# Performance work log

Measured on AMD Instinct MI355X. Metric: run time of the kernel, lower is better.

The kernel has to match this reference:

```python
import jax, jax.numpy as jnp
import numpy as np

B, S, K = 64, 80, 32          # patients, max visits, codes per visit
V, E, H, L = 10000, 256, 512, 128  # vocab, embed, hidden, latent


def setup_inputs() -> dict:
    key = jax.random.key(0)
    ks = jax.random.split(key, 9)
    input_sequence = jax.random.randint(ks[0], (B, S, K), 0, V)
    length = jax.random.randint(ks[1], (B,), 1, S + 1)  # valid lengths >= 1
    sc = 0.05
    embedding_weight = jax.random.normal(ks[2], (V, E), jnp.float32) * sc
    Wi = jax.random.normal(ks[3], (3 * H, E), jnp.float32) * sc   # W_ih (r,z,n)
    Wh = jax.random.normal(ks[4], (3 * H, H), jnp.float32) * sc   # W_hh (r,z,n)
    bi = jax.random.normal(ks[5], (3 * H,), jnp.float32) * sc
    bh = jax.random.normal(ks[6], (3 * H,), jnp.float32) * sc
    W_lat = jax.random.normal(ks[7], (L, H), jnp.float32) * sc
    b_lat = jax.random.normal(ks[8], (L,), jnp.float32) * sc
    return dict(input_sequence=input_sequence, length=length,
                embedding_weight=embedding_weight, Wi=Wi, Wh=Wh, bi=bi, bh=bh,
                W_lat=W_lat, b_lat=b_lat)


def _encode(input_sequence, length, embedding_weight, Wi, Wh, bi, bh, W_lat, b_lat):
    b, s, k = input_sequence.shape
    v, e = embedding_weight.shape
    h = Wh.shape[1]
    # torch.sort(length, descending=True) -> batch reorder (output stays sorted!)
    sorted_idx = jnp.argsort(-length)
    sorted_len = length[sorted_idx]
    seq = input_sequence[sorted_idx]
    # multi-hot scatter: duplicates collapse to 1, matching torch scatter_(dim=2, val=1)
    onehot = jnp.zeros((b, s, v), jnp.float32)
    onehot = onehot.at[jnp.arange(b)[:, None, None],
                       jnp.arange(s)[None, :, None], seq].set(1.0)
    onehot = onehot.at[:, :, 0].set(0.0)  # code 0 is padding
    emb = jnp.tanh(jnp.einsum('bsv,ve->bse', onehot, embedding_weight))  # [B,S,E]
    # packed GRU == masked scan: hidden frozen once t >= length
    mask = jnp.arange(s)[None, :] < sorted_len[:, None]  # [B,S]
    xs = jnp.swapaxes(emb, 0, 1)   # [S,B,E]
    ms = jnp.swapaxes(mask, 0, 1)  # [S,B]

    def step(hprev, xm):
        x, m = xm
        gi = x @ Wi.T + bi        # [B,3H]
        gh = hprev @ Wh.T + bh    # [B,3H]
        i_r, i_z, i_n = jnp.split(gi, 3, axis=-1)
        h_r, h_z, h_n = jnp.split(gh, 3, axis=-1)
        r = jax.nn.sigmoid(i_r + h_r)
        z = jax.nn.sigmoid(i_z + h_z)
        n = jnp.tanh(i_n + r * h_n)
        hnew = (1.0 - z) * n + z * hprev
        return jnp.where(m[:, None], hnew, hprev), None

    h0 = jnp.zeros((b, h), jnp.float32)
    hT, _ = jax.lax.scan(step, h0, (xs, ms))  # last valid hidden per sequence
    return jnp.tanh(hT @ W_lat.T + b_lat)     # [B,L], in sorted order


def reference(input_sequence, length, embedding_weight, Wi, Wh, bi, bh, W_lat, b_lat):
    return _encode(input_sequence, length, embedding_weight, Wi, Wh, bi, bh, W_lat, b_lat)
```

## Files before the change

kernel.cpp:

```cpp
#include <hip/hip_runtime.h>
#include <cmath>

typedef _Float16 f16;
typedef _Float16 f16x8 __attribute__((ext_vector_type(8)));
typedef float f32x4 __attribute__((ext_vector_type(4)));
typedef unsigned int u32x4 __attribute__((ext_vector_type(4)));

#define B 64
#define S 80
#define KC 32
#define EDIM 256
#define HDIM 512
#define G3 1536
#define LDIM 128

#define NG 8
#define PG 8
#define NJ 16
#define CPB 32

#define OFF_PCNT  (NG * NJ * 64)
#define OFF_XCD   (OFF_PCNT + NG * 64)
#define OFF_TEST  (OFF_XCD + NG * NJ)
#define OFF_FAIL  (OFF_TEST + NG * NJ * 64)
#define SYNC_TOTAL (OFF_FAIL + NG)

__device__ __forceinline__ unsigned int ld_u32c(const unsigned int* p, bool l2) {
    unsigned int v;
    if (l2) {
        asm volatile("global_load_dword %0, %1, off sc0\n\ts_waitcnt vmcnt(0)"
                     : "=v"(v) : "v"(p) : "memory");
    } else {
        v = __hip_atomic_load(p, __ATOMIC_RELAXED, __HIP_MEMORY_SCOPE_AGENT);
    }
    return v;
}
__device__ __forceinline__ void st_u32c(unsigned int* p, unsigned int v, bool l2) {
    if (l2) {
        asm volatile("global_store_dword %0, %1, off sc0" :: "v"(p), "v"(v) : "memory");
    } else {
        __hip_atomic_store(p, v, __ATOMIC_RELAXED, __HIP_MEMORY_SCOPE_AGENT);
    }
}

__global__ __launch_bounds__(256) void emb_kernel(const int* __restrict__ seq,
                                                  const float* __restrict__ Ew,
                                                  unsigned short* __restrict__ emb16) {
    int bs = blockIdx.x;
    __shared__ int codes[KC];
    __shared__ int valid[KC];
    int tid = threadIdx.x;
    if (tid < KC) codes[tid] = seq[bs * KC + tid];
    __syncthreads();
    if (tid < KC) {
        int c = codes[tid];
        int v = (c != 0);
        for (int i = 0; i < tid; ++i)
            if (codes[i] == c) v = 0;
        valid[tid] = v;
    }
    __syncthreads();
    float acc = 0.f;
    for (int j = 0; j < KC; ++j) {
        if (valid[j]) acc += Ew[codes[j] * EDIM + tid];
    }
    emb16[bs * EDIM + tid] = __builtin_bit_cast(unsigned short, (f16)tanhf(acc));
}

__global__ __launch_bounds__(256) void gi_gemm16(
        const unsigned short* __restrict__ wi16,
        const unsigned short* __restrict__ emb16,
        const float* __restrict__ bi,
        unsigned short* __restrict__ gi16) {
    __shared__ __align__(16) f16 At[64][256];
    __shared__ __align__(16) f16 Bt[64][256];
    const int m0 = blockIdx.x * 64;
    const int n0 = blockIdx.y * 64;
    const int tid = threadIdx.x;
    #pragma unroll
    for (int i = 0; i < 8; ++i) {
        int ci = tid + i * 256;
        int row = ci >> 5, c = ci & 31;
        int sc = c ^ (row & 7);
        *(f32x4*)&At[row][sc * 8] =
            *(const f32x4*)(wi16 + (size_t)(n0 + row) * EDIM + c * 8);
        *(f32x4*)&Bt[row][sc * 8] =
            *(const f32x4*)(emb16 + (size_t)(m0 + row) * EDIM + c * 8);
    }
    __syncthreads();
    const int wv = tid >> 6, ln = tid & 63;
    const int lr = ln & 15, hi = ln >> 4;
    const int arow = wv * 16 + lr;
    f32x4 acc[4] = {};
    #pragma unroll
    for (int ks = 0; ks < 8; ++ks) {
        int ca = (ks * 4 + hi) ^ (arow & 7);
        f32x4 av = *(const f32x4*)&At[arow][ca * 8];
        #pragma unroll
        for (int vt = 0; vt < 4; ++vt) {
            int brow = vt * 16 + lr;
            int cb = (ks * 4 + hi) ^ (brow & 7);
            f32x4 bv = *(const f32x4*)&Bt[brow][cb * 8];
            acc[vt] = __builtin_amdgcn_mfma_f32_16x16x32_f16(
                __builtin_bit_cast(f16x8, av), __builtin_bit_cast(f16x8, bv),
                acc[vt], 0, 0, 0);
        }
    }
    const int gate0 = n0 + wv * 16 + hi * 4;
    float4 bv4 = *(const float4*)(bi + gate0);
    #pragma unroll
    for (int vt = 0; vt < 4; ++vt) {
        int vis = m0 + vt * 16 + lr;
        union { unsigned short u[4]; unsigned long long ll; } pk;
        pk.u[0] = __builtin_bit_cast(unsigned short, (f16)(acc[vt][0] + bv4.x));
        pk.u[1] = __builtin_bit_cast(unsigned short, (f16)(acc[vt][1] + bv4.y));
        pk.u[2] = __builtin_bit_cast(unsigned short, (f16)(acc[vt][2] + bv4.z));
        pk.u[3] = __builtin_bit_cast(unsigned short, (f16)(acc[vt][3] + bv4.w));
        *(unsigned long long*)(gi16 + (size_t)vis * G3 + gate0) = pk.ll;
    }
}

__global__ __launch_bounds__(256) void init_kernel(const int* __restrict__ len,
                                                   const float* __restrict__ Wi,
                                                   const float* __restrict__ Wh,
                                                   int* __restrict__ rank,
                                                   unsigned int* __restrict__ sync,
                                                   unsigned int* __restrict__ hz,
                                                   unsigned short* __restrict__ wi16,
                                                   unsigned short* __restrict__ wh16) {
    int idx = blockIdx.x * 256 + threadIdx.x;
    if (idx < 16384) { hz[idx] = 0u; hz[16384 + idx] = 0u; }
    for (int o = idx; o < SYNC_TOTAL; o += 32768) sync[o] = 0u;
    for (int o = idx; o < G3 * EDIM; o += 32768)
        wi16[o] = __builtin_bit_cast(unsigned short, (f16)Wi[o]);
    for (int o = idx; o < G3 * HDIM; o += 32768)
        wh16[o] = __builtin_bit_cast(unsigned short, (f16)Wh[o]);
    if (blockIdx.x == 0 && threadIdx.x < B) {
        int t = threadIdx.x;
        int lb = len[t];
        int r = 0;
        for (int i = 0; i < B; ++i) {
            int li = len[i];
            r += (li > lb) || (li == lb && i < t);
        }
        rank[t] = r;
    }
}

__global__ __launch_bounds__(256, 1) void gru_persist(
        const unsigned short* __restrict__ gi16,
        const unsigned short* __restrict__ wh16,
        const float* __restrict__ bh, const int* __restrict__ len,
        unsigned short* __restrict__ h0f, unsigned short* __restrict__ h1f,
        unsigned short* __restrict__ hout,
        unsigned int* __restrict__ sync) {
    const int g     = blockIdx.x;
    const int slice = blockIdx.y;
    const int tid   = threadIdx.x;
    const int wv    = tid >> 6;
    const int ln    = tid & 63;
    const int c0    = slice * CPB;

    __shared__ __align__(16) f32x4 wlds[96 * 65];
    __shared__ __align__(16) f16 hsb[64][16][8];
    __shared__ float ghl[3][CPB][16];
    __shared__ unsigned int ids_sh[NJ];
    __shared__ unsigned int fail_sh;

    for (int c = tid; c < 64 * 8; c += 256)
        *(float4*)&hsb[c >> 3][8 + (c & 7)][0] = make_float4(0.f, 0.f, 0.f, 0.f);

    #pragma unroll
    for (int i = 0; i < 24; ++i) {
        int idx = tid + i * 256;
        int row = idx >> 6, slot = idx & 63;
        int gate = row >> 5, lr = row & 31;
        wlds[row * 65 + slot] =
            *(const f32x4*)(wh16 + (size_t)(gate * HDIM + c0 + lr) * HDIM + slot * 8);
    }

    unsigned int* gflags = sync + (size_t)(g * NJ) * 64;
    unsigned int* pcnt   = sync + OFF_PCNT + g * 64;
    unsigned int* xcdrow = sync + OFF_XCD + g * NJ;
    unsigned int* town   = sync + OFF_TEST + (g * NJ + slice) * 64;
    unsigned int* tpeer  = sync + OFF_TEST + (g * NJ + ((slice + 1) & (NJ - 1))) * 64;
    unsigned int* failw  = sync + OFF_FAIL + g;

    auto l3bar = [&](unsigned int target) {
        if (tid == 0) {
            asm volatile("s_waitcnt vmcnt(0)" ::: "memory");
            __hip_atomic_fetch_add(pcnt, 1u, __ATOMIC_RELAXED, __HIP_MEMORY_SCOPE_AGENT);
            while (__hip_atomic_load(pcnt, __ATOMIC_RELAXED, __HIP_MEMORY_SCOPE_AGENT) < target)
                __builtin_amdgcn_s_sleep(1);
        }
        __syncthreads();
    };

    unsigned int myxcc;
    asm volatile("s_getreg_b32 %0, hwreg(HW_REG_XCC_ID)" : "=s"(myxcc));
    myxcc &= 0xFu;
    if (tid == 0)
        __hip_atomic_store(xcdrow + slice, myxcc, __ATOMIC_RELAXED, __HIP_MEMORY_SCOPE_AGENT);
    l3bar(NJ);
    if (tid < NJ)
        ids_sh[tid] = __hip_atomic_load(xcdrow + tid, __ATOMIC_RELAXED, __HIP_MEMORY_SCOPE_AGENT);
    __syncthreads();
    bool same_xcd = true;
    #pragma unroll
    for (int i = 1; i < NJ; ++i) same_xcd &= (ids_sh[i] == ids_sh[0]);

    bool l2m = false;
    if (same_xcd) {
        const unsigned int M1 = 0xA5A50000u + (unsigned)slice;
        const unsigned int M2 = 0x5A5A0000u + (unsigned)slice;
        const unsigned int P1 = 0xA5A50000u + (unsigned)((slice + 1) & (NJ - 1));
        const unsigned int P2 = 0x5A5A0000u + (unsigned)((slice + 1) & (NJ - 1));
        unsigned int r1 = 0, r2 = 0;
        if (tid == 0) st_u32c(town, M1, true);
        l3bar(2 * NJ);
        if (tid == 0) r1 = ld_u32c(tpeer, true);
        l3bar(3 * NJ);
        if (tid == 0) st_u32c(town, M2, true);
        l3bar(4 * NJ);
        if (tid == 0) {
            r2 = ld_u32c(tpeer, true);
            if (r1 != P1 || r2 != P2)
                __hip_atomic_fetch_or(failw, 1u, __ATOMIC_RELAXED, __HIP_MEMORY_SCOPE_AGENT);
        }
        l3bar(5 * NJ);
        if (tid == 0)
            fail_sh = __hip_atomic_load(failw, __ATOMIC_RELAXED, __HIP_MEMORY_SCOPE_AGENT);
        __syncthreads();
        l2m = (fail_sh == 0u);
    }

    const int pat  = tid >> 4;
    const int cp   = tid & 15;
    const int colw = cp * 2;
    const int colg = c0 + colw;
    const int fb   = g * PG + pat;
    float2 bhp[3] = {};
    const unsigned short* gi_b = gi16;
    int flen = 0;
    if (tid < 128) {
        #pragma unroll
        for (int gg = 0; gg < 3; ++gg)
            bhp[gg] = *(const float2*)(bh + gg * HDIM + colg);
        gi_b = gi16 + (size_t)fb * S * G3;
        flen = len[fb];
    }
    int Lg = 0;
    #pragma unroll
    for (int i = 0; i < PG; ++i) Lg = max(Lg, len[g * PG + i]);

    unsigned short* hb0 = h0f + (size_t)g * PG * HDIM;
    unsigned short* hb1 = h1f + (size_t)g * PG * HDIM;

    const int g0p = tid & 7, g0k = tid >> 3;
    const int g1k = g0k + 32;

    unsigned int giC[3] = {};
    if (tid < 128) {
        #pragma unroll
        for (int gg = 0; gg < 3; ++gg)
            giC[gg] = *(const unsigned int*)(gi_b + gg * HDIM + colg);
    }

    unsigned int lastH = 0;

    #pragma unroll 1
    for (int t = 0; t < Lg; ++t) {
        const unsigned short* src = (t & 1) ? hb1 : hb0;
        unsigned short*       dst = (t & 1) ? hb0 : hb1;

        {
            const unsigned short* p0 = src + g0p * HDIM + g0k * 8;
            const unsigned short* p1 = src + g0p * HDIM + g1k * 8;
            if (l2m) {
                u32x4 v0, v1;
                asm volatile(
                    "global_load_dwordx4 %0, %2, off sc0\n\t"
                    "global_load_dwordx4 %1, %3, off sc0\n\t"
                    "s_waitcnt vmcnt(0)"
                    : "=v"(v0), "=v"(v1) : "v"(p0), "v"(p1) : "memory");
                *(u32x4*)&hsb[g0k][g0p][0] = v0;
                *(u32x4*)&hsb[g1k][g0p][0] = v1;
            } else {
                u32x4 v0, v1;
                #pragma unroll
                for (int i = 0; i < 4; ++i) {
                    v0[i] = __hip_atomic_load((const unsigned int*)p0 + i,
                                              __ATOMIC_RELAXED, __HIP_MEMORY_SCOPE_AGENT);
                    v1[i] = __hip_atomic_load((const unsigned int*)p1 + i,
                                              __ATOMIC_RELAXED, __HIP_MEMORY_SCOPE_AGENT);
                }
                *(u32x4*)&hsb[g0k][g0p][0] = v0;
                *(u32x4*)&hsb[g1k][g0p][0] = v1;
            }
        }
        __syncthreads();

        if (wv < 3) {
            const int lr = ln & 15, hi = ln >> 4;
            #pragma unroll
            for (int cc = 0; cc < 2; ++cc) {
                const f32x4* wrow = &wlds[(wv * 32 + cc * 16 + lr) * 65 + hi];
                f32x4 a0 = (f32x4){0.f, 0.f, 0.f, 0.f};
                f32x4 a1 = (f32x4){0.f, 0.f, 0.f, 0.f};
                #pragma unroll
                for (int ks = 0; ks < 8; ++ks) {
                    f32x4 av = wrow[ks * 4];
                    f32x4 bv = *(const f32x4*)&hsb[ks * 4 + hi][lr][0];
                    a0 = __builtin_amdgcn_mfma_f32_16x16x32_f16(
                        __builtin_bit_cast(f16x8, av),
                        __builtin_bit_cast(f16x8, bv), a0, 0, 0, 0);
                }
                #pragma unroll
                for (int ks = 8; ks < 16; ++ks) {
                    f32x4 av = wrow[ks * 4];
                    f32x4 bv = *(const f32x4*)&hsb[ks * 4 + hi][lr][0];
                    a1 = __builtin_amdgcn_mfma_f32_16x16x32_f16(
                        __builtin_bit_cast(f16x8, av),
                        __builtin_bit_cast(f16x8, bv), a1, 0, 0, 0);
                }
                #pragma unroll
                for (int i = 0; i < 4; ++i)
                    ghl[wv][cc * 16 + hi * 4 + i][lr] = a0[i] + a1[i];
            }
        }
        __syncthreads();

        if (tid < 128) {
            unsigned int hold2 =
                *(const unsigned int*)&hsb[colg >> 3][pat][colg & 7];
            union { f16 h[2]; unsigned int v; } pk, hv;
            hv.v = hold2;
            #pragma unroll
            for (int i = 0; i < 2; ++i) {
                float sr = ghl[0][colw + i][pat];
                float sz = ghl[1][colw + i][pat];
                float sn = ghl[2][colw + i][pat];
                f16 g2[2];
                *(unsigned int*)g2 = giC[0];
                float gr = (float)g2[i];
                *(unsigned int*)g2 = giC[1];
                float gz = (float)g2[i];
                *(unsigned int*)g2 = giC[2];
                float gn = (float)g2[i];
                float bb = i ? bhp[0].y : bhp[0].x;
                float bz = i ? bhp[1].y : bhp[1].x;
                float bn = i ? bhp[2].y : bhp[2].x;
                float r  = 1.f / (1.f + expf(-(gr + sr + bb)));
                float z  = 1.f / (1.f + expf(-(gz + sz + bz)));
                float nn = tanhf(gn + r * (sn + bn));
                float hold = (float)hv.h[i];
                float hnew = (t < flen) ? ((1.f - z) * nn + z * hold) : hold;
                pk.h[i] = (f16)hnew;
            }
            lastH = pk.v;
            unsigned short* d = dst + pat * HDIM + colg;
            if (l2m) {
                asm volatile("global_store_dword %0, %1, off sc0"
                             :: "v"(d), "v"(pk.v) : "memory");
            } else {
                __hip_atomic_store((unsigned int*)d, pk.v,
                                   __ATOMIC_RELAXED, __HIP_MEMORY_SCOPE_AGENT);
            }
        }
        asm volatile("s_waitcnt vmcnt(0)" ::: "memory");
        __syncthreads();
        if (tid == 0) st_u32c(gflags + slice * 64, (unsigned)(t + 1), l2m);

        unsigned int giN[3] = {};
        if (tid < 128) {
            int tn = (t + 1 < S) ? (t + 1) : (S - 1);
            const unsigned short* gp = gi_b + (size_t)tn * G3;
            #pragma unroll
            for (int gg = 0; gg < 3; ++gg)
                giN[gg] = *(const unsigned int*)(gp + gg * HDIM + colg);
        }

        if (tid < NJ) {
            unsigned int* f = gflags + tid * 64;
            while (ld_u32c(f, l2m) < (unsigned)(t + 1))
                __builtin_amdgcn_s_sleep(1);
        }
        __syncthreads();

        giC[0] = giN[0]; giC[1] = giN[1]; giC[2] = giN[2];
    }

    if (tid < 128)
        *(unsigned int*)(hout + (size_t)fb * HDIM + colg) = lastH;
}

__global__ __launch_bounds__(128) void final_kernel(const unsigned short* __restrict__ h,
                                                    const float* __restrict__ Wl,
                                                    const float* __restrict__ bl,
                                                    const int* __restrict__ rank,
                                                    float* __restrict__ out) {
    int b = blockIdx.x;
    int l = threadIdx.x;
    __shared__ float hsh[HDIM];
    for (int i = l; i < HDIM; i += LDIM)
        hsh[i] = (float)__builtin_bit_cast(f16, h[(size_t)b * HDIM + i]);
    __syncthreads();
    float acc = bl[l];
    for (int k = 0; k < HDIM; ++k) acc += hsh[k] * Wl[(size_t)l * HDIM + k];
    out[(size_t)rank[b] * LDIM + l] = tanhf(acc);
}

extern "C" void kernel_launch(void* const* d_in, const int* in_sizes, int n_in,
                              void* d_out, int out_size, void* d_ws, size_t ws_size,
                              hipStream_t stream) {
    const int*   seq = (const int*)d_in[0];
    const int*   len = (const int*)d_in[1];
    const float* Ew  = (const float*)d_in[2];
    const float* Wi  = (const float*)d_in[3];
    const float* Wh  = (const float*)d_in[4];
    const float* bi  = (const float*)d_in[5];
    const float* bh  = (const float*)d_in[6];
    const float* Wl  = (const float*)d_in[7];
    const float* bl  = (const float*)d_in[8];
    float* out = (float*)d_out;

    unsigned short* ws16 = (unsigned short*)d_ws;
    unsigned short* emb16 = ws16;
    unsigned short* gi16  = emb16 + (size_t)B * S * EDIM;
    unsigned short* wi16  = gi16 + (size_t)B * S * G3;
    unsigned short* wh16  = wi16 + (size_t)G3 * EDIM;
    unsigned short* h0f   = wh16 + (size_t)G3 * HDIM;
    unsigned short* h1f   = h0f + (size_t)B * HDIM;
    unsigned short* hout  = h1f + (size_t)B * HDIM;
    int*   rank = (int*)(hout + (size_t)B * HDIM);
    unsigned int* sync = (unsigned int*)(rank + B);

    emb_kernel<<<B * S, 256, 0, stream>>>(seq, Ew, emb16);
    init_kernel<<<128, 256, 0, stream>>>(len, Wi, Wh, rank, sync,
                                         (unsigned int*)h0f, wi16, wh16);
    gi_gemm16<<<dim3(B * S / 64, G3 / 64), 256, 0, stream>>>(wi16, emb16, bi, gi16);

    gru_persist<<<dim3(NG, NJ), 256, 0, stream>>>(gi16, wh16, bh, len,
                                                  h0f, h1f, hout, sync);
    final_kernel<<<B, LDIM, 0, stream>>>(hout, Wl, bl, rank, out);
}
```

Baseline: 323.2 us.

## Split GRU columns across twice as many blocks, keep Wh in registers

```diff
diff --git a/kernel.cpp b/kernel.cpp
--- a/kernel.cpp
+++ b/kernel.cpp
@@ -16,8 +16,8 @@
 
 #define NG 8
 #define PG 8
-#define NJ 16
-#define CPB 32
+#define NJ 32
+#define CPB 16
 
 #define OFF_PCNT  (NG * NJ * 64)
 #define OFF_XCD   (OFF_PCNT + NG * 64)
@@ -161,23 +161,27 @@
     const int ln    = tid & 63;
     const int c0    = slice * CPB;
 
-    __shared__ __align__(16) f32x4 wlds[96 * 65];
     __shared__ __align__(16) f16 hsb[64][16][8];
-    __shared__ float ghl[3][CPB][16];
+    __shared__ float ghl[3][16][18];
     __shared__ unsigned int ids_sh[NJ];
     __shared__ unsigned int fail_sh;
 
     for (int c = tid; c < 64 * 8; c += 256)
         *(float4*)&hsb[c >> 3][8 + (c & 7)][0] = make_float4(0.f, 0.f, 0.f, 0.f);
 
-    #pragma unroll
-    for (int i = 0; i < 24; ++i) {
-        int idx = tid + i * 256;
-        int row = idx >> 6, slot = idx & 63;
-        int gate = row >> 5, lr = row & 31;
-        wlds[row * 65 + slot] =
-            *(const f32x4*)(wh16 + (size_t)(gate * HDIM + c0 + lr) * HDIM + slot * 8);
-    }
+    f32x4 af[16];
+    if (wv < 3) {
+        const unsigned short* wrow =
+            wh16 + (size_t)(wv * HDIM + c0 + (ln & 15)) * HDIM + (ln >> 4) * 8;
+        #pragma unroll
+        for (int ks = 0; ks < 16; ++ks)
+            af[ks] = *(const f32x4*)(wrow + ks * 32);
+    } else {
+        #pragma unroll
+        for (int ks = 0; ks < 16; ++ks) af[ks] = (f32x4){0.f, 0.f, 0.f, 0.f};
+    }
+    #pragma unroll
+    for (int ks = 0; ks < 16; ++ks) asm volatile("" : "+v"(af[ks]));
 
     unsigned int* gflags = sync + (size_t)(g * NJ) * 64;
     unsigned int* pcnt   = sync + OFF_PCNT + g * 64;
@@ -234,15 +238,14 @@
         l2m = (fail_sh == 0u);
     }
 
-    const int pat  = tid >> 4;
-    const int cp   = tid & 15;
-    const int colw = cp * 2;
+    const int pat  = tid >> 3;
+    const int colw = (tid & 7) * 2;
     const int colg = c0 + colw;
     const int fb   = g * PG + pat;
     float2 bhp[3] = {};
     const unsigned short* gi_b = gi16;
     int flen = 0;
-    if (tid < 128) {
+    if (tid < 64) {
         #pragma unroll
         for (int gg = 0; gg < 3; ++gg)
             bhp[gg] = *(const float2*)(bh + gg * HDIM + colg);
@@ -260,7 +263,7 @@
     const int g1k = g0k + 32;
 
     unsigned int giC[3] = {};
-    if (tid < 128) {
+    if (tid < 64) {
         #pragma unroll
         for (int gg = 0; gg < 3; ++gg)
             giC[gg] = *(const unsigned int*)(gi_b + gg * HDIM + colg);
@@ -301,52 +304,41 @@
         __syncthreads();
 
         if (wv < 3) {
-            const int lr = ln & 15, hi = ln >> 4;
+            f32x4 a0 = (f32x4){0.f, 0.f, 0.f, 0.f};
+            f32x4 a1 = (f32x4){0.f, 0.f, 0.f, 0.f};
             #pragma unroll
-            for (int cc = 0; cc < 2; ++cc) {
-                const f32x4* wrow = &wlds[(wv * 32 + cc * 16 + lr) * 65 + hi];
-                f32x4 a0 = (f32x4){0.f, 0.f, 0.f, 0.f};
-                f32x4 a1 = (f32x4){0.f, 0.f, 0.f, 0.f};
-                #pragma unroll
-                for (int ks = 0; ks < 8; ++ks) {
-                    f32x4 av = wrow[ks * 4];
-                    f32x4 bv = *(const f32x4*)&hsb[ks * 4 + hi][lr][0];
-                    a0 = __builtin_amdgcn_mfma_f32_16x16x32_f16(
-                        __builtin_bit_cast(f16x8, av),
-                        __builtin_bit_cast(f16x8, bv), a0, 0, 0, 0);
-                }
-                #pragma unroll
-                for (int ks = 8; ks < 16; ++ks) {
-                    f32x4 av = wrow[ks * 4];
-                    f32x4 bv = *(const f32x4*)&hsb[ks * 4 + hi][lr][0];
-                    a1 = __builtin_amdgcn_mfma_f32_16x16x32_f16(
-                        __builtin_bit_cast(f16x8, av),
-                        __builtin_bit_cast(f16x8, bv), a1, 0, 0, 0);
-                }
-                #pragma unroll
-                for (int i = 0; i < 4; ++i)
-                    ghl[wv][cc * 16 + hi * 4 + i][lr] = a0[i] + a1[i];
+            for (int ks = 0; ks < 8; ++ks) {
+                f32x4 bv = *(const f32x4*)&hsb[ks * 4 + (ln >> 4)][ln & 15][0];
+                a0 = __builtin_amdgcn_mfma_f32_16x16x32_f16(
+                    __builtin_bit_cast(f16x8, af[ks]),
+                    __builtin_bit_cast(f16x8, bv), a0, 0, 0, 0);
             }
+            #pragma unroll
+            for (int ks = 8; ks < 16; ++ks) {
+                f32x4 bv = *(const f32x4*)&hsb[ks * 4 + (ln >> 4)][ln & 15][0];
+                a1 = __builtin_amdgcn_mfma_f32_16x16x32_f16(
+                    __builtin_bit_cast(f16x8, af[ks]),
+                    __builtin_bit_cast(f16x8, bv), a1, 0, 0, 0);
+            }
+            #pragma unroll
+            for (int i = 0; i < 4; ++i)
+                ghl[wv][(ln >> 4) * 4 + i][ln & 15] = a0[i] + a1[i];
         }
         __syncthreads();
 
-        if (tid < 128) {
+        if (tid < 64) {
             unsigned int hold2 =
                 *(const unsigned int*)&hsb[colg >> 3][pat][colg & 7];
-            union { f16 h[2]; unsigned int v; } pk, hv;
+            union { f16 h[2]; unsigned int v; } pk, hv, gp;
             hv.v = hold2;
             #pragma unroll
             for (int i = 0; i < 2; ++i) {
                 float sr = ghl[0][colw + i][pat];
                 float sz = ghl[1][colw + i][pat];
                 float sn = ghl[2][colw + i][pat];
-                f16 g2[2];
-                *(unsigned int*)g2 = giC[0];
-                float gr = (float)g2[i];
-                *(unsigned int*)g2 = giC[1];
-                float gz = (float)g2[i];
-                *(unsigned int*)g2 = giC[2];
-                float gn = (float)g2[i];
+                gp.v = giC[0]; float gr = (float)gp.h[i];
+                gp.v = giC[1]; float gz = (float)gp.h[i];
+                gp.v = giC[2]; float gn = (float)gp.h[i];
                 float bb = i ? bhp[0].y : bhp[0].x;
                 float bz = i ? bhp[1].y : bhp[1].x;
                 float bn = i ? bhp[2].y : bhp[2].x;
@@ -366,31 +358,22 @@
                 __hip_atomic_store((unsigned int*)d, pk.v,
                                    __ATOMIC_RELAXED, __HIP_MEMORY_SCOPE_AGENT);
             }
-        }
-        asm volatile("s_waitcnt vmcnt(0)" ::: "memory");
-        __syncthreads();
-        if (tid == 0) st_u32c(gflags + slice * 64, (unsigned)(t + 1), l2m);
-
-        unsigned int giN[3] = {};
-        if (tid < 128) {
+            asm volatile("s_waitcnt vmcnt(0)" ::: "memory");
+            if (tid == 0) st_u32c(gflags + slice * 64, (unsigned)(t + 1), l2m);
             int tn = (t + 1 < S) ? (t + 1) : (S - 1);
-            const unsigned short* gp = gi_b + (size_t)tn * G3;
+            const unsigned short* gpp = gi_b + (size_t)tn * G3;
             #pragma unroll
             for (int gg = 0; gg < 3; ++gg)
-                giN[gg] = *(const unsigned int*)(gp + gg * HDIM + colg);
-        }
-
-        if (tid < NJ) {
-            unsigned int* f = gflags + tid * 64;
+                giC[gg] = *(const unsigned int*)(gpp + gg * HDIM + colg);
+        } else if (tid < 64 + NJ) {
+            unsigned int* f = gflags + (tid - 64) * 64;
             while (ld_u32c(f, l2m) < (unsigned)(t + 1))
                 __builtin_amdgcn_s_sleep(1);
         }
         __syncthreads();
-
-        giC[0] = giN[0]; giC[1] = giN[1]; giC[2] = giN[2];
-    }
-
-    if (tid < 128)
+    }
+
+    if (tid < 64)
         *(unsigned int*)(hout + (size_t)fb * HDIM + colg) = lastH;
 }
 
```

New measurement: 308.1 us. 1.05x faster.
